# Kernel optimization log

Measured on AMD Instinct MI355X. Metric: run time of the kernel, lower is better.

The kernel has to match this reference:

```python
import jax, jax.numpy as jnp
import numpy as np

N_NODES = 50000
N_EDGES = 625000
D = 128          # hidden_dim
H = 8            # num_heads
DH = D // H      # head_dim
L = 4            # num_layers
F_IN = 64        # in_channels
G = 64           # num graphs
BETA = 1.0
EPS = 1e-5       # layernorm eps


def _seg_softmax(s, idx, n):
    # softmax of s over segments defined by idx (segments present in idx are never empty)
    m = jax.ops.segment_max(s, idx, num_segments=n)
    e = jnp.exp(s - m[idx])
    d = jax.ops.segment_sum(e, idx, num_segments=n)
    return e / d[idx]


def _ln(x, s, b):
    mu = jnp.mean(x, axis=-1, keepdims=True)
    var = jnp.var(x, axis=-1, keepdims=True)
    return (x - mu) / jnp.sqrt(var + EPS) * s + b


def _forward(x, edge_index, batch, node_W, node_b, cW1, cb1, cW2, cb2,
             qW, qb, kW, kb, vW, vb, oW, ob, bW, bb,
             f1W, f1b, f2W, f2b, n1s, n1b, n2s, n2b,
             outW1, outb1, outW2, outb2):
    N = x.shape[0]
    src, tgt = edge_index[0], edge_index[1]
    h = x @ node_W + node_b                              # [N, D]
    for l in range(L):
        # ---- dynamic curvature (attention-approximated Wasserstein) ----
        h_src, h_tgt = h[src], h[tgt]                    # [E, D]
        sim = jnp.sum(h_src * h_tgt, axis=-1) * BETA     # [E]
        alpha = _seg_softmax(sim, tgt, N)                # segment softmax over tgt
        dist = jnp.linalg.norm(h_src - h_tgt, axis=-1)   # [E]
        agg = jax.ops.segment_sum(alpha * dist, tgt, num_segments=N)
        curv = 1.0 - agg[tgt] / jnp.maximum(dist, 1e-6)  # [E]
        ce = jax.nn.relu(curv[:, None] @ cW1 + cb1) @ cW2 + cb2  # [E, D]
        # ---- CurvphormerLayer ----
        xn = _ln(h, n1s[l], n1b[l])
        q = (xn @ qW[l] + qb[l]).reshape(N, H, DH)
        k = (xn @ kW[l] + kb[l]).reshape(N, H, DH)
        v = (xn @ vW[l] + vb[l]).reshape(N, H, DH)
        scores = jnp.sum(q[src] * k[tgt], axis=-1) / (DH ** 0.5)  # [E, H]
        scores = scores + ce @ bW[l] + bb[l]                       # curvature bias
        probs = _seg_softmax(scores, tgt, N)                       # [E, H]
        msgs = (probs[..., None] * v[tgt]).reshape(-1, D)          # [E, D]
        aggm = jax.ops.segment_sum(msgs, src, num_segments=N)     # scatter to src
        h = h + (aggm @ oW[l] + ob[l])
        xn2 = _ln(h, n2s[l], n2b[l])
        h = h + (jax.nn.relu(xn2 @ f1W[l] + f1b[l]) @ f2W[l] + f2b[l])
    # ---- mean pool per graph ----
    counts = jnp.maximum(jax.ops.segment_sum(jnp.ones((N,), h.dtype), batch, num_segments=G), 1.0)
    g = jax.ops.segment_sum(h, batch, num_segments=G) / counts[:, None]
    return jax.nn.relu(g @ outW1 + outb1) @ outW2 + outb2


def setup_inputs() -> dict:
    keys = iter(jax.random.split(jax.random.key(0), 32))
    p = lambda shape, s=0.02: jax.random.normal(next(keys), shape, jnp.float32) * s
    x = jax.random.normal(next(keys), (N_NODES, F_IN), jnp.float32)
    edge_index = jax.random.randint(next(keys), (2, N_EDGES), 0, N_NODES)
    batch = jnp.sort(jax.random.randint(next(keys), (N_NODES,), 0, G))
    inp = {
        "x": x, "edge_index": edge_index, "batch": batch,
        "node_W": p((F_IN, D)), "node_b": p((D,)),
        "cW1": p((1, D)), "cb1": p((D,)), "cW2": p((D, D)), "cb2": p((D,)),
        "qW": p((L, D, D)), "qb": p((L, D)),
        "kW": p((L, D, D)), "kb": p((L, D)),
        "vW": p((L, D, D)), "vb": p((L, D)),
        "oW": p((L, D, D)), "ob": p((L, D)),
        "bW": p((L, D, H)), "bb": p((L, H)),
        "f1W": p((L, D, 4 * D)), "f1b": p((L, 4 * D)),
        "f2W": p((L, 4 * D, D)), "f2b": p((L, D)),
        "n1s": jnp.ones((L, D), jnp.float32), "n1b": jnp.zeros((L, D), jnp.float32),
        "n2s": jnp.ones((L, D), jnp.float32), "n2b": jnp.zeros((L, D), jnp.float32),
        "outW1": p((D, D // 2)), "outb1": p((D // 2,)),
        "outW2": p((D // 2, 1)), "outb2": p((1,)),
    }
    return inp


def reference(x, edge_index, batch, node_W, node_b, cW1, cb1, cW2, cb2,
              qW, qb, kW, kb, vW, vb, oW, ob, bW, bb,
              f1W, f1b, f2W, f2b, n1s, n1b, n2s, n2b,
              outW1, outb1, outW2, outb2):
    return _forward(x, edge_index, batch, node_W, node_b, cW1, cb1, cW2, cb2,
                    qW, qb, kW, kb, vW, vb, oW, ob, bW, bb,
                    f1W, f1b, f2W, f2b, n1s, n1b, n2s, n2b,
                    outW1, outb1, outW2, outb2)
```

## Files before the change

kernel.cpp:

```cpp
#include <hip/hip_runtime.h>

#define NN 50000
#define NE 625000
#define DD 128
#define HH 8
#define DHH 16
#define NL 4
#define FIN 64
#define NG 64
#define LN_EPS 1e-5f
#define NSEG 129
#define NT32 1563
#define NT64 782
#define NT4 12500
#define NBS 196
#define HLP 132

typedef __bf16 bf16x8_t __attribute__((ext_vector_type(8)));
typedef unsigned short ushort8_t __attribute__((ext_vector_type(8)));
typedef float f32x4_t __attribute__((ext_vector_type(4)));
union BF8 { ushort8_t u; bf16x8_t b; };

__device__ __forceinline__ void fma4(float4& a, float s, float4 w) {
  a.x = fmaf(s, w.x, a.x); a.y = fmaf(s, w.y, a.y);
  a.z = fmaf(s, w.z, a.z); a.w = fmaf(s, w.w, a.w);
}
__device__ __forceinline__ unsigned short f2bf(float f) {
  unsigned u = __float_as_uint(f);
  unsigned r = ((u >> 16) & 1u) + 0x7FFFu;
  return (unsigned short)((u + r) >> 16);
}
__device__ __forceinline__ float bf2f(unsigned short u) {
  return __uint_as_float((unsigned)u << 16);
}

__device__ __forceinline__ void ln_tile_bf32(const float* __restrict__ h, int nb,
                                             const float* __restrict__ sc,
                                             const float* __restrict__ bi,
                                             ushort* xbf) {
  int tid = threadIdx.x;
  int r = tid >> 4, l16 = tid & 15;
  int nr = nb + r; if (nr >= NN) nr = NN - 1;
  const float* hp = h + (size_t)nr * DD + l16 * 8;
  float4 a0 = *(const float4*)hp;
  float4 a1 = *(const float4*)(hp + 4);
  float sum = a0.x + a0.y + a0.z + a0.w + a1.x + a1.y + a1.z + a1.w;
  float sq  = a0.x*a0.x + a0.y*a0.y + a0.z*a0.z + a0.w*a0.w
            + a1.x*a1.x + a1.y*a1.y + a1.z*a1.z + a1.w*a1.w;
#pragma unroll
  for (int off = 8; off >= 1; off >>= 1) {
    sum += __shfl_xor(sum, off, 64);
    sq  += __shfl_xor(sq,  off, 64);
  }
  float mu   = sum * (1.0f / DD);
  float var  = sq * (1.0f / DD) - mu * mu;
  float rstd = rsqrtf(var + LN_EPS);
  int d0 = l16 * 8;
  float4 s0 = *(const float4*)(sc + d0), s1 = *(const float4*)(sc + d0 + 4);
  float4 b0 = *(const float4*)(bi + d0), b1 = *(const float4*)(bi + d0 + 4);
  ushort8_t u;
  u[0] = f2bf((a0.x - mu) * rstd * s0.x + b0.x);
  u[1] = f2bf((a0.y - mu) * rstd * s0.y + b0.y);
  u[2] = f2bf((a0.z - mu) * rstd * s0.z + b0.z);
  u[3] = f2bf((a0.w - mu) * rstd * s0.w + b0.w);
  u[4] = f2bf((a1.x - mu) * rstd * s1.x + b1.x);
  u[5] = f2bf((a1.y - mu) * rstd * s1.y + b1.y);
  u[6] = f2bf((a1.z - mu) * rstd * s1.z + b1.z);
  u[7] = f2bf((a1.w - mu) * rstd * s1.w + b1.w);
  int off = (r * 256 + l16 * 16) ^ ((r & 7) << 4);
  *(ushort8_t*)((char*)xbf + off) = u;
}

__global__ __launch_bounds__(256) void k_node_proj(const float* __restrict__ x,
                                                   const float* __restrict__ W,
                                                   const float* __restrict__ b,
                                                   float* __restrict__ h) {
  __shared__ float Wl[FIN * DD];
  __shared__ float xt[32][FIN];
  int tid = threadIdx.x;
  int nb = blockIdx.x * 32;
  for (int i = tid * 4; i < FIN * DD; i += 1024)
    *(float4*)&Wl[i] = *(const float4*)(W + i);
  for (int i = tid * 4; i < 32 * FIN; i += 1024) {
    int row = i >> 6, cc = i & 63;
    int node = nb + row; if (node >= NN) node = NN - 1;
    *(float4*)&xt[row][cc] = *(const float4*)(x + (size_t)node * FIN + cc);
  }
  __syncthreads();
  int c4 = (tid & 31) * 4;
  int r0 = (tid >> 5) * 4;
  float4 bv = *(const float4*)(b + c4);
  float4 a0 = bv, a1 = bv, a2 = bv, a3 = bv;
  for (int k = 0; k < FIN; k++) {
    float4 wv = *(const float4*)&Wl[k * DD + c4];
    fma4(a0, xt[r0][k], wv);
    fma4(a1, xt[r0 + 1][k], wv);
// ... 130 lines not shown
    den += __shfl_xor(den, off, 64);
    nd  += __shfl_xor(nd,  off, 64);
  }
  float av = den > 0.f ? nd / den : 0.f;
  int hh = lane & 7;
  int eidx = lane >> 3;
  const ushort8_t* kp = (const ushort8_t*)(k + (size_t)node * DD + hh * DHH);
  ushort8_t k0 = kp[0], k1 = kp[1];
  float m = -3.4e38f, ssum = 0.f;
  for (int i = rs + eidx; i < re; i += 8) {
    int e = eid_t[i];
    int s = src_s[e];
    float dd = dist[e];
    const ushort8_t* qp = (const ushort8_t*)(q + (size_t)s * DD + hh * DHH);
    ushort8_t q0 = qp[0], q1 = qp[1];
    float curv = 1.0f - av / fmaxf(dd, 1e-6f);
    int lo = 0, hi = DD;
    while (lo < hi) { int mid = (lo + hi) >> 1; if (bp[mid] < curv) lo = mid + 1; else hi = mid; }
    float bias = fmaf(lsl[lo * HH + hh], curv, lin[lo * HH + hh]);
    float dot = 0.f;
#pragma unroll
    for (int jj = 0; jj < 8; jj++) dot = fmaf(bf2f(q0[jj]), bf2f(k0[jj]), dot);
#pragma unroll
    for (int jj = 0; jj < 8; jj++) dot = fmaf(bf2f(q1[jj]), bf2f(k1[jj]), dot);
    float sc = dot * 0.25f + bias;
    escore[e * HH + hh] = sc;
    float mn = fmaxf(m, sc);
    ssum = ssum * expf(m - mn) + expf(sc - mn);
    m = mn;
  }
#pragma unroll
  for (int off = 8; off <= 32; off <<= 1) {
    float m2 = __shfl_xor(m, off, 64);
    float s2 = __shfl_xor(ssum, off, 64);
    float M = fmaxf(m, m2);
    ssum = ssum * expf(m - M) + s2 * expf(m2 - M);
    m = M;
  }
  float inv = ssum > 0.f ? 1.0f / ssum : 0.f;
  for (int i = rs + eidx; i < re; i += 8) {
    size_t idx = (size_t)eid_t[i] * HH + hh;
    float sc = escore[idx];
    escore[idx] = expf(sc - m) * inv;
  }
}

__global__ __launch_bounds__(256) void k_agg(const int* __restrict__ tgt_s,
    const int* __restrict__ rowstart,
    const float* __restrict__ escore,
    const ushort* __restrict__ v, ushort* __restrict__ aggmb) {
  int wave = (blockIdx.x * 256 + threadIdx.x) >> 6;
  int lane = threadIdx.x & 63;
  int rs = rowstart[wave], re = rowstart[wave + 1];
  int hh = lane >> 3;
  int d = lane * 2;
  float a0 = 0.f, a1 = 0.f;
  int i = rs;
  for (; i + 4 <= re; i += 4) {
    int t0 = tgt_s[i], t1 = tgt_s[i + 1], t2 = tgt_s[i + 2], t3 = tgt_s[i + 3];
    float p0 = escore[(i    ) * HH + hh];
    float p1 = escore[(i + 1) * HH + hh];
    float p2 = escore[(i + 2) * HH + hh];
    float p3 = escore[(i + 3) * HH + hh];
    ushort2 v0 = *(const ushort2*)(v + (size_t)t0 * DD + d);
    ushort2 v1 = *(const ushort2*)(v + (size_t)t1 * DD + d);
    ushort2 v2 = *(const ushort2*)(v + (size_t)t2 * DD + d);
    ushort2 v3 = *(const ushort2*)(v + (size_t)t3 * DD + d);
    a0 = fmaf(p0, bf2f(v0.x), a0); a1 = fmaf(p0, bf2f(v0.y), a1);
    a0 = fmaf(p1, bf2f(v1.x), a0); a1 = fmaf(p1, bf2f(v1.y), a1);
    a0 = fmaf(p2, bf2f(v2.x), a0); a1 = fmaf(p2, bf2f(v2.y), a1);
    a0 = fmaf(p3, bf2f(v3.x), a0); a1 = fmaf(p3, bf2f(v3.y), a1);
  }
  for (; i < re; i++) {
    int t = tgt_s[i];
    float prob = escore[i * HH + hh];
    ushort2 vv = *(const ushort2*)(v + (size_t)t * DD + d);
    a0 = fmaf(prob, bf2f(vv.x), a0);
    a1 = fmaf(prob, bf2f(vv.y), a1);
  }
  ushort2 o; o.x = f2bf(a0); o.y = f2bf(a1);
  *(ushort2*)(aggmb + (size_t)wave * DD + d) = o;
}

__global__ __launch_bounds__(512) void k_attn_ffn(const ushort* __restrict__ aggmb,
    const ushort* __restrict__ oT_l, const float* __restrict__ ob_l,
    const float* __restrict__ n2s_l, const float* __restrict__ n2b_l,
    const ushort* __restrict__ f1T_l, const float* __restrict__ f1b_l,
    const ushort* __restrict__ f2T_l, const float* __restrict__ f2b_l,
    float* __restrict__ h,
    int do_qkv,
    const float* __restrict__ n1s_n, const float* __restrict__ n1b_n,
    const ushort* __restrict__ qkvT_n,
    const float* __restrict__ qb_n, const float* __restrict__ kb_n, const float* __restrict__ vb_n,
    ushort* __restrict__ q, ushort* __restrict__ kk, ushort* __restrict__ v) {
  __shared__ float hL[64 * HLP];
  __shared__ __align__(16) char ubuf[64 * 128 * 2];
  char* xb = ubuf;
  char* tb = ubuf;
  int nb = blockIdx.x * 64;
  int tid = threadIdx.x;
  int lane = tid & 63, w = tid >> 6;
  int g = lane >> 4, c = lane & 15;
  int colb = w * 16;
  int xr = (c & 7) << 4;
  {
    float4 obv = *(const float4*)(ob_l + colb + g * 4);
    const ushort* wp = oT_l + (size_t)(colb + c) * DD + g * 8;
    BF8 b0, b1, b2, b3;
    b0.u = *(const ushort8_t*)(wp);
    b1.u = *(const ushort8_t*)(wp + 32);
    b2.u = *(const ushort8_t*)(wp + 64);
    b3.u = *(const ushort8_t*)(wp + 96);
#pragma unroll
    for (int nt = 0; nt < 4; nt++) {
      int node = nb + nt * 16 + c;
      int na = node < NN ? node : NN - 1;
      const ushort* ap = aggmb + (size_t)na * DD + g * 8;
      BF8 a0, a1, a2, a3;
      a0.u = *(const ushort8_t*)(ap);
      a1.u = *(const ushort8_t*)(ap + 32);
      a2.u = *(const ushort8_t*)(ap + 64);
      a3.u = *(const ushort8_t*)(ap + 96);
      f32x4_t acc = {obv.x, obv.y, obv.z, obv.w};
      acc = __builtin_amdgcn_mfma_f32_16x16x32_bf16(b0.b, a0.b, acc, 0, 0, 0);
      acc = __builtin_amdgcn_mfma_f32_16x16x32_bf16(b1.b, a1.b, acc, 0, 0, 0);
      acc = __builtin_amdgcn_mfma_f32_16x16x32_bf16(b2.b, a2.b, acc, 0, 0, 0);
      acc = __builtin_amdgcn_mfma_f32_16x16x32_bf16(b3.b, a3.b, acc, 0, 0, 0);
      float4 hv = *(const float4*)(h + (size_t)na * DD + colb + g * 4);
      hv.x += acc[0]; hv.y += acc[1]; hv.z += acc[2]; hv.w += acc[3];
      *(float4*)&hL[(nt * 16 + c) * HLP + colb + g * 4] = hv;
    }
  }
  __syncthreads();
  {
    int l16 = tid & 15;
    int d0 = l16 * 8;
    float4 s0 = *(const float4*)(n2s_l + d0), s1 = *(const float4*)(n2s_l + d0 + 4);
    float4 bb0 = *(const float4*)(n2b_l + d0), bb1 = *(const float4*)(n2b_l + d0 + 4);
#pragma unroll
    for (int p = 0; p < 2; p++) {
      int r = p * 32 + (tid >> 4);
      const float* hp = &hL[r * HLP + d0];
      float4 a0 = *(const float4*)hp;
      float4 a1 = *(const float4*)(hp + 4);
      float sum = a0.x + a0.y + a0.z + a0.w + a1.x + a1.y + a1.z + a1.w;
      float sq  = a0.x*a0.x + a0.y*a0.y + a0.z*a0.z + a0.w*a0.w
                + a1.x*a1.x + a1.y*a1.y + a1.z*a1.z + a1.w*a1.w;
#pragma unroll
      for (int off = 8; off >= 1; off >>= 1) {
        sum += __shfl_xor(sum, off, 64);
        sq  += __shfl_xor(sq,  off, 64);
      }
      float mu   = sum * (1.0f / DD);
      float var  = sq * (1.0f / DD) - mu * mu;
      float rstd = rsqrtf(var + LN_EPS);
      ushort8_t u;
      u[0] = f2bf((a0.x - mu) * rstd * s0.x + bb0.x);
      u[1] = f2bf((a0.y - mu) * rstd * s0.y + bb0.y);
      u[2] = f2bf((a0.z - mu) * rstd * s0.z + bb0.z);
      u[3] = f2bf((a0.w - mu) * rstd * s0.w + bb0.w);
      u[4] = f2bf((a1.x - mu) * rstd * s1.x + bb1.x);
      u[5] = f2bf((a1.y - mu) * rstd * s1.y + bb1.y);
      u[6] = f2bf((a1.z - mu) * rstd * s1.z + bb1.z);
      u[7] = f2bf((a1.w - mu) * rstd * s1.w + bb1.w);
      int off = (r * 256 + l16 * 16) ^ ((r & 7) << 4);
      *(ushort8_t*)(xb + off) = u;
    }
  }
  __syncthreads();
  BF8 a[4][4];
#pragma unroll
  for (int nt = 0; nt < 4; nt++)
#pragma unroll
    for (int kt = 0; kt < 4; kt++)
      a[nt][kt].u = *(ushort8_t*)(xb + (((nt * 16 + c) * 256 + kt * 64 + g * 16) ^ xr));
  __syncthreads();
  float4 bv2 = *(const float4*)(f2b_l + colb + g * 4);
  f32x4_t o0 = {bv2.x, bv2.y, bv2.z, bv2.w};
  f32x4_t o1 = o0, o2 = o0, o3 = o0;
#pragma unroll
  for (int ch = 0; ch < 4; ch++) {
    if (ch) __syncthreads();
    {
      int col = ch * 128 + w * 16;
      float4 bv = *(const float4*)(f1b_l + col + g * 4);
      f32x4_t ac0 = {bv.x, bv.y, bv.z, bv.w};
      f32x4_t ac1 = ac0, ac2 = ac0, ac3 = ac0;
      const ushort* wp = f1T_l + (size_t)(col + c) * DD + g * 8;
#pragma unroll
      for (int kt = 0; kt < 4; kt++) {
        BF8 b; b.u = *(const ushort8_t*)(wp + kt * 32);
        ac0 = __builtin_amdgcn_mfma_f32_16x16x32_bf16(b.b, a[0][kt].b, ac0, 0, 0, 0);
        ac1 = __builtin_amdgcn_mfma_f32_16x16x32_bf16(b.b, a[1][kt].b, ac1, 0, 0, 0);
        ac2 = __builtin_amdgcn_mfma_f32_16x16x32_bf16(b.b, a[2][kt].b, ac2, 0, 0, 0);
        ac3 = __builtin_amdgcn_mfma_f32_16x16x32_bf16(b.b, a[3][kt].b, ac3, 0, 0, 0);
      }
      int colL = (w * 16 + g * 4) * 2;
      {
        int row = c;
        ushort4 o4; o4.x = f2bf(fmaxf(ac0[0], 0.f)); o4.y = f2bf(fmaxf(ac0[1], 0.f));
        o4.z = f2bf(fmaxf(ac0[2], 0.f)); o4.w = f2bf(fmaxf(ac0[3], 0.f));
        *(ushort4*)(tb + ((row * 256 + colL) ^ ((row & 7) << 4))) = o4;
      }
      {
        int row = 16 + c;
        ushort4 o4; o4.x = f2bf(fmaxf(ac1[0], 0.f)); o4.y = f2bf(fmaxf(ac1[1], 0.f));
        o4.z = f2bf(fmaxf(ac1[2], 0.f)); o4.w = f2bf(fmaxf(ac1[3], 0.f));
        *(ushort4*)(tb + ((row * 256 + colL) ^ ((row & 7) << 4))) = o4;
      }
      {
        int row = 32 + c;
        ushort4 o4; o4.x = f2bf(fmaxf(ac2[0], 0.f)); o4.y = f2bf(fmaxf(ac2[1], 0.f));
        o4.z = f2bf(fmaxf(ac2[2], 0.f)); o4.w = f2bf(fmaxf(ac2[3], 0.f));
        *(ushort4*)(tb + ((row * 256 + colL) ^ ((row & 7) << 4))) = o4;
      }
      {
        int row = 48 + c;
        ushort4 o4; o4.x = f2bf(fmaxf(ac3[0], 0.f)); o4.y = f2bf(fmaxf(ac3[1], 0.f));
        o4.z = f2bf(fmaxf(ac3[2], 0.f)); o4.w = f2bf(fmaxf(ac3[3], 0.f));
        *(ushort4*)(tb + ((row * 256 + colL) ^ ((row & 7) << 4))) = o4;
      }
    }
    __syncthreads();
    const ushort* wp2 = f2T_l + (size_t)(colb + c) * 512 + ch * 128 + g * 8;
#pragma unroll
    for (int kt = 0; kt < 4; kt++) {
      BF8 b; b.u = *(const ushort8_t*)(wp2 + kt * 32);
      BF8 t0; t0.u = *(ushort8_t*)(tb + (((c) * 256 + kt * 64 + g * 16) ^ xr));
      BF8 t1; t1.u = *(ushort8_t*)(tb + (((16 + c) * 256 + kt * 64 + g * 16) ^ xr));
      BF8 t2; t2.u = *(ushort8_t*)(tb + (((32 + c) * 256 + kt * 64 + g * 16) ^ xr));
      BF8 t3; t3.u = *(ushort8_t*)(tb + (((48 + c) * 256 + kt * 64 + g * 16) ^ xr));
      o0 = __builtin_amdgcn_mfma_f32_16x16x32_bf16(b.b, t0.b, o0, 0, 0, 0);
      o1 = __builtin_amdgcn_mfma_f32_16x16x32_bf16(b.b, t1.b, o1, 0, 0, 0);
      o2 = __builtin_amdgcn_mfma_f32_16x16x32_bf16(b.b, t2.b, o2, 0, 0, 0);
      o3 = __builtin_amdgcn_mfma_f32_16x16x32_bf16(b.b, t3.b, o3, 0, 0, 0);
    }
  }
  {
    float* lp = &hL[c * HLP + colb + g * 4];
    float4 hv = *(const float4*)lp;
    hv.x += o0[0]; hv.y += o0[1]; hv.z += o0[2]; hv.w += o0[3];
    *(float4*)lp = hv;
    int node = nb + c;
    if (node < NN) *(float4*)(h + (size_t)node * DD + colb + g * 4) = hv;
  }
  {
    float* lp = &hL[(16 + c) * HLP + colb + g * 4];
    float4 hv = *(const float4*)lp;
    hv.x += o1[0]; hv.y += o1[1]; hv.z += o1[2]; hv.w += o1[3];
    *(float4*)lp = hv;
    int node = nb + 16 + c;
    if (node < NN) *(float4*)(h + (size_t)node * DD + colb + g * 4) = hv;
  }
  {
    float* lp = &hL[(32 + c) * HLP + colb + g * 4];
    float4 hv = *(const float4*)lp;
    hv.x += o2[0]; hv.y += o2[1]; hv.z += o2[2]; hv.w += o2[3];
    *(float4*)lp = hv;
    int node = nb + 32 + c;
    if (node < NN) *(float4*)(h + (size_t)node * DD + colb + g * 4) = hv;
  }
  {
    float* lp = &hL[(48 + c) * HLP + colb + g * 4];
    float4 hv = *(const float4*)lp;
    hv.x += o3[0]; hv.y += o3[1]; hv.z += o3[2]; hv.w += o3[3];
    *(float4*)lp = hv;
    int node = nb + 48 + c;
    if (node < NN) *(float4*)(h + (size_t)node * DD + colb + g * 4) = hv;
  }
  if (!do_qkv) return;
  __syncthreads();
  {
    int l16 = tid & 15;
    int d0 = l16 * 8;
    float4 s0 = *(const float4*)(n1s_n + d0), s1 = *(const float4*)(n1s_n + d0 + 4);
    float4 bb0 = *(const float4*)(n1b_n + d0), bb1 = *(const float4*)(n1b_n + d0 + 4);
#pragma unroll
    for (int p = 0; p < 2; p++) {
      int r = p * 32 + (tid >> 4);
      const float* hp = &hL[r * HLP + d0];
      float4 a0 = *(const float4*)hp;
      float4 a1 = *(const float4*)(hp + 4);
      float sum = a0.x + a0.y + a0.z + a0.w + a1.x + a1.y + a1.z + a1.w;
      float sq  = a0.x*a0.x + a0.y*a0.y + a0.z*a0.z + a0.w*a0.w
                + a1.x*a1.x + a1.y*a1.y + a1.z*a1.z + a1.w*a1.w;
#pragma unroll
      for (int off = 8; off >= 1; off >>= 1) {
        sum += __shfl_xor(sum, off, 64);
        sq  += __shfl_xor(sq,  off, 64);
      }
      float mu   = sum * (1.0f / DD);
      float var  = sq * (1.0f / DD) - mu * mu;
      float rstd = rsqrtf(var + LN_EPS);
      ushort8_t u;
      u[0] = f2bf((a0.x - mu) * rstd * s0.x + bb0.x);
      u[1] = f2bf((a0.y - mu) * rstd * s0.y + bb0.y);
      u[2] = f2bf((a0.z - mu) * rstd * s0.z + bb0.z);
      u[3] = f2bf((a0.w - mu) * rstd * s0.w + bb0.w);
      u[4] = f2bf((a1.x - mu) * rstd * s1.x + bb1.x);
      u[5] = f2bf((a1.y - mu) * rstd * s1.y + bb1.y);
      u[6] = f2bf((a1.z - mu) * rstd * s1.z + bb1.z);
      u[7] = f2bf((a1.w - mu) * rstd * s1.w + bb1.w);
      int off = (r * 256 + l16 * 16) ^ ((r & 7) << 4);
      *(ushort8_t*)(xb + off) = u;
    }
  }
  __syncthreads();
  BF8 aq[4][4];
#pragma unroll
  for (int nt = 0; nt < 4; nt++)
#pragma unroll
    for (int kt = 0; kt < 4; kt++)
      aq[nt][kt].u = *(ushort8_t*)(xb + (((nt * 16 + c) * 256 + kt * 64 + g * 16) ^ xr));
#pragma unroll
  for (int ti = 0; ti < 3; ti++) {
    int t = w * 3 + ti;
    int m = t >> 3;
    int colq = (t & 7) * 16;
    const float* bias = (m == 0 ? qb_n : (m == 1 ? kb_n : vb_n));
    float4 bv = *(const float4*)(bias + colq + g * 4);
    f32x4_t ac0 = {bv.x, bv.y, bv.z, bv.w};
    f32x4_t ac1 = ac0, ac2 = ac0, ac3 = ac0;
    const ushort* wp = qkvT_n + (size_t)(m * DD + colq + c) * DD + g * 8;
#pragma unroll
    for (int kt = 0; kt < 4; kt++) {
      BF8 b; b.u = *(const ushort8_t*)(wp + kt * 32);
      ac0 = __builtin_amdgcn_mfma_f32_16x16x32_bf16(b.b, aq[0][kt].b, ac0, 0, 0, 0);
      ac1 = __builtin_amdgcn_mfma_f32_16x16x32_bf16(b.b, aq[1][kt].b, ac1, 0, 0, 0);
      ac2 = __builtin_amdgcn_mfma_f32_16x16x32_bf16(b.b, aq[2][kt].b, ac2, 0, 0, 0);
      ac3 = __builtin_amdgcn_mfma_f32_16x16x32_bf16(b.b, aq[3][kt].b, ac3, 0, 0, 0);
    }
    ushort* out = (m == 0 ? q : (m == 1 ? kk : v));
    {
      int node = nb + c;
      if (node < NN) {
        ushort4 o; o.x = f2bf(ac0[0]); o.y = f2bf(ac0[1]); o.z = f2bf(ac0[2]); o.w = f2bf(ac0[3]);
        *(ushort4*)(out + (size_t)node * DD + colq + g * 4) = o;
      }
    }
    {
      int node = nb + 16 + c;
      if (node < NN) {
        ushort4 o; o.x = f2bf(ac1[0]); o.y = f2bf(ac1[1]); o.z = f2bf(ac1[2]); o.w = f2bf(ac1[3]);
        *(ushort4*)(out + (size_t)node * DD + colq + g * 4) = o;
      }
    }
    {
      int node = nb + 32 + c;
      if (node < NN) {
        ushort4 o; o.x = f2bf(ac2[0]); o.y = f2bf(ac2[1]); o.z = f2bf(ac2[2]); o.w = f2bf(ac2[3]);
        *(ushort4*)(out + (size_t)node * DD + colq + g * 4) = o;
      }
    }
    {
      int node = nb + 48 + c;
      if (node < NN) {
        ushort4 o; o.x = f2bf(ac3[0]); o.y = f2bf(ac3[1]); o.z = f2bf(ac3[2]); o.w = f2bf(ac3[3]);
        *(ushort4*)(out + (size_t)node * DD + colq + g * 4) = o;
      }
    }
  }
}

__global__ __launch_bounds__(256) void k_zero(int* __restrict__ cnt, int* __restrict__ cur,
                                              int* __restrict__ cnt_t, int* __restrict__ cur_t,
                                              int* __restrict__ gstart, int* __restrict__ gend,
                                              float* __restrict__ gpool) {
  int i = blockIdx.x * 256 + threadIdx.x;
  if (i < NN) { cnt[i] = 0; cur[i] = 0; cnt_t[i] = 0; cur_t[i] = 0; }
  if (i < NG) { gstart[i] = 0; gend[i] = 0; }
  if (i < NG * DD) gpool[i] = 0.f;
}

__global__ void k_hist2(const int* __restrict__ src, const int* __restrict__ tgt,
                        int* __restrict__ cnt, int* __restrict__ cnt_t) {
  int e = blockIdx.x * 256 + threadIdx.x;
  if (e < NE) {
    atomicAdd(cnt + src[e], 1);
    atomicAdd(cnt_t + tgt[e], 1);
  }
}

__global__ __launch_bounds__(256) void k_scan_blk2(const int* __restrict__ cnt,
                                                   const int* __restrict__ cnt_t,
                                                   int* __restrict__ bsum, int* __restrict__ bsum_t) {
  __shared__ int red[256];
  int arr = blockIdx.x >= NBS ? 1 : 0;
  int b = blockIdx.x - arr * NBS;
  const int* c = arr ? cnt_t : cnt;
  int* bs = arr ? bsum_t : bsum;
  int tid = threadIdx.x;
  int idx = b * 256 + tid;
  red[tid] = (idx < NN) ? c[idx] : 0;
  __syncthreads();
  for (int off = 128; off >= 1; off >>= 1) {
    if (tid < off) red[tid] += red[tid + off];
    __syncthreads();
  }
  if (tid == 0) bs[b] = red[0];
}

__global__ __launch_bounds__(256) void k_scan_top2(const int* __restrict__ bsum,
                                                   const int* __restrict__ bsum_t,
                                                   int* __restrict__ boff, int* __restrict__ boff_t,
                                                   int* __restrict__ rowstart, int* __restrict__ rowstart_t) {
  __shared__ int ps[256];
  int arr = blockIdx.x;
  const int* bs = arr ? bsum_t : bsum;
  int* bo = arr ? boff_t : boff;
  int* rsN = arr ? rowstart_t : rowstart;
  int t = threadIdx.x;
  int v = (t < NBS) ? bs[t] : 0;
  ps[t] = v;
  __syncthreads();
  for (int off = 1; off < 256; off <<= 1) {
    int x = (t >= off) ? ps[t - off] : 0;
    __syncthreads();
    ps[t] += x;
    __syncthreads();
  }
  bo[t] = ps[t] - v;
  if (t == 255) rsN[NN] = ps[255];
}

__global__ __launch_bounds__(256) void k_scan_fin2(const int* __restrict__ cnt,
                                                   const int* __restrict__ cnt_t,
                                                   const int* __restrict__ boff, const int* __restrict__ boff_t,
                                                   int* __restrict__ rowstart, int* __restrict__ rowstart_t) {
  __shared__ int ps[256];
  int arr = blockIdx.x >= NBS ? 1 : 0;
  int b = blockIdx.x - arr * NBS;
  const int* c = arr ? cnt_t : cnt;
  const int* bo = arr ? boff_t : boff;
  int* rs = arr ? rowstart_t : rowstart;
  int t = threadIdx.x;
  int idx = b * 256 + t;
  int v = (idx < NN) ? c[idx] : 0;
  ps[t] = v;
  __syncthreads();
  for (int off = 1; off < 256; off <<= 1) {
    int x = (t >= off) ? ps[t - off] : 0;
    __syncthreads();
    ps[t] += x;
    __syncthreads();
  }
  if (idx < NN) rs[idx] = bo[b] + ps[t] - v;
}

__global__ void k_fill(const int* __restrict__ src, const int* __restrict__ tgt,
                       const int* __restrict__ rowstart,
                       int* __restrict__ cur, int* __restrict__ src_s, int* __restrict__ tgt_s) {
  int e = blockIdx.x * 256 + threadIdx.x;
  if (e >= NE) return;
// ... 37 lines not shown
  idx -= SZ1;
  if (idx < SZF) { wt_one(f1W, f1T, idx, DD, 512, DD * 512); return; }
  idx -= SZF;
  if (idx < SZF) { wt_one(f2W, f2T, idx, 512, DD, 512 * DD); return; }
}

__global__ __launch_bounds__(64) void k_mbias_par(const float* __restrict__ cW2, const float* __restrict__ cb2,
                                                  const float* __restrict__ bW, const float* __restrict__ bb,
                                                  float* __restrict__ M, float* __restrict__ base) {
  int bid = blockIdx.x;
  int l = bid >> 7, d = bid & 127;
  int lane = threadIdx.x;
  int hh = lane >> 3, j0 = lane & 7;
  const float* bWl = bW + (size_t)l * DD * HH;
  float acc = 0.f;
#pragma unroll
  for (int t = 0; t < 16; t++) {
    int k = j0 + t * 8;
    acc = fmaf(cW2[d * DD + k], bWl[k * HH + hh], acc);
  }
#pragma unroll
  for (int off = 1; off <= 4; off <<= 1) acc += __shfl_xor(acc, off, 64);
  if (j0 == 0) M[(size_t)l * DD * HH + d * HH + hh] = acc;
  if (d == 0) {
    float bacc = 0.f;
#pragma unroll
    for (int t = 0; t < 16; t++) {
      int k = j0 + t * 8;
      bacc = fmaf(cb2[k], bWl[k * HH + hh], bacc);
    }
#pragma unroll
    for (int off = 1; off <= 4; off <<= 1) bacc += __shfl_xor(bacc, off, 64);
    if (j0 == 0) base[l * HH + hh] = bacc + bb[l * HH + hh];
  }
}

__global__ __launch_bounds__(128) void k_bp(const float* __restrict__ cW1, const float* __restrict__ cb1,
                                            float* __restrict__ bpg, int* __restrict__ posg) {
  __shared__ float x[DD], bp[DD];
  int tid = threadIdx.x;
  float c1v = cW1[tid], cbv = cb1[tid];
  x[tid] = (c1v == 0.f) ? __builtin_inff() : (-cbv / c1v);
  __syncthreads();
  float xv = x[tid]; int p = 0;
  for (int j = 0; j < DD; j++) {
    float xj = x[j];
    if (xj < xv || (xj == xv && j < tid)) p++;
  }
  bp[p] = xv;
  posg[tid] = p;
  __syncthreads();
  bpg[tid] = bp[tid];
}

__global__ __launch_bounds__(64) void k_pwl_tab(const float* __restrict__ cW1, const float* __restrict__ cb1,
    const int* __restrict__ posg, const float* __restrict__ Mb, const float* __restrict__ basel,
    float* __restrict__ slopeg, float* __restrict__ interg) {
  int bid = blockIdx.x;
  int l = bid / NSEG, s = bid - l * NSEG;
  int lane = threadIdx.x;
  int hh = lane >> 3, j0 = lane & 7;
  const float* M = Mb + (size_t)l * DD * HH;
  float sl = 0.f, in = 0.f;
#pragma unroll
  for (int t = 0; t < 16; t++) {
    int d = j0 + t * 8;
    float cv = cW1[d], cbv = cb1[d];
    int p = posg[d];
    bool act = (cv == 0.f) ? (cbv > 0.f) : ((cv > 0.f) ? (p < s) : (p >= s));
    float m = act ? M[d * HH + hh] : 0.f;
    sl = fmaf(cv, m, sl);
    in = fmaf(cbv, m, in);
  }
#pragma unroll
  for (int off = 1; off <= 4; off <<= 1) {
    sl += __shfl_xor(sl, off, 64);
    in += __shfl_xor(in, off, 64);
  }
  if (j0 == 0) {
    size_t o = (size_t)l * NSEG * HH + s * HH + hh;
    slopeg[o] = sl;
    interg[o] = in + basel[l * HH + hh];
  }
}

__global__ void k_bounds(const int* __restrict__ batch, int* __restrict__ gstart, int* __restrict__ gend) {
  int n = blockIdx.x * 256 + threadIdx.x;
  if (n >= NN) return;
  int b = batch[n];
  if (n == 0 || batch[n - 1] != b) gstart[b] = n;
  if (n == NN - 1 || batch[n + 1] != b) gend[b] = n + 1;
}

__global__ __launch_bounds__(256) void k_pool_part(const float* __restrict__ h,
    const int* __restrict__ batch, float* __restrict__ gpool) {
  int tid = threadIdx.x;
  int d = tid & 127, sub = tid >> 7;
  int n0 = blockIdx.x * 256;
  int nend = n0 + 256; if (nend > NN) nend = NN;
  float run = 0.f; int gcur = -1;
  for (int n = n0 + sub; n < nend; n += 2) {
    int g = batch[n];
    if (g != gcur) {
      if (gcur >= 0) atomicAdd(gpool + (size_t)gcur * DD + d, run);
      run = 0.f; gcur = g;
    }
    run += h[(size_t)n * DD + d];
  }
  if (gcur >= 0) atomicAdd(gpool + (size_t)gcur * DD + d, run);
}

__global__ __launch_bounds__(256) void k_head(const float* __restrict__ gpool,
    const int* __restrict__ gstart, const int* __restrict__ gend,
    const float* __restrict__ W1, const float* __restrict__ b1,
    const float* __restrict__ W2, const float* __restrict__ b2, float* __restrict__ out) {
  __shared__ float mid[NG * 64];
  int tid = threadIdx.x;
  for (int idx = tid; idx < NG * 64; idx += 256) {
    int g = idx >> 6, j = idx & 63;
    int cnt = gend[g] - gstart[g]; if (cnt < 1) cnt = 1;
    float rc = 1.0f / (float)cnt;
    float acc = 0.f;
    for (int d = 0; d < DD; d++) acc = fmaf(gpool[g * DD + d], W1[d * 64 + j], acc);
    mid[idx] = fmaxf(fmaf(acc, rc, b1[j]), 0.f);
  }
  __syncthreads();
  if (tid < NG) {
    float acc = b2[0];
    for (int j = 0; j < 64; j++) acc = fmaf(mid[tid * 64 + j], W2[j], acc);
    out[tid] = acc;
  }
}

extern "C" void kernel_launch(void* const* d_in, const int* in_sizes, int n_in,
                              void* d_out, int out_size, void* d_ws, size_t ws_size,
                              hipStream_t stream) {
  const float* x      = (const float*)d_in[0];
  const int*   ei     = (const int*)d_in[1];
  const int*   batch  = (const int*)d_in[2];
  const float* node_W = (const float*)d_in[3];
  const float* node_b = (const float*)d_in[4];
  const float* cW1    = (const float*)d_in[5];
  const float* cb1    = (const float*)d_in[6];
  const float* cW2    = (const float*)d_in[7];
  const float* cb2    = (const float*)d_in[8];
  const float* qW     = (const float*)d_in[9];
  const float* qb     = (const float*)d_in[10];
  const float* kW     = (const float*)d_in[11];
  const float* kb     = (const float*)d_in[12];
  const float* vW     = (const float*)d_in[13];
  const float* vb     = (const float*)d_in[14];
  const float* oW     = (const float*)d_in[15];
  const float* ob     = (const float*)d_in[16];
  const float* bW     = (const float*)d_in[17];
  const float* bb     = (const float*)d_in[18];
  const float* f1W    = (const float*)d_in[19];
  const float* f1b    = (const float*)d_in[20];
  const float* f2W    = (const float*)d_in[21];
  const float* f2b    = (const float*)d_in[22];
  const float* n1s    = (const float*)d_in[23];
  const float* n1b    = (const float*)d_in[24];
  const float* n2s    = (const float*)d_in[25];
  const float* n2b    = (const float*)d_in[26];
  const float* outW1  = (const float*)d_in[27];
  const float* outb1  = (const float*)d_in[28];
  const float* outW2  = (const float*)d_in[29];
  const float* outb2  = (const float*)d_in[30];

  const int* src = ei;
  const int* tgt = ei + NE;

  char* wp = (char*)d_ws;
  auto alloc = [&](size_t bytes) { void* p = (void*)wp; wp += (bytes + 255) & ~(size_t)255; return p; };
  float*    h       = (float*)alloc((size_t)NN * DD * 4);
  ushort*   q       = (ushort*)alloc((size_t)NN * DD * 2);
  ushort*   kk      = (ushort*)alloc((size_t)NN * DD * 2);
  ushort*   v       = (ushort*)alloc((size_t)NN * DD * 2);
  ushort*   aggmb   = (ushort*)alloc((size_t)NN * DD * 2);
  float*    sim     = (float*)alloc((size_t)NE * 4);
  float*    dist    = (float*)alloc((size_t)NE * 4);
  float*    escore  = (float*)alloc((size_t)NE * HH * 4);
  float*    Mb      = (float*)alloc((size_t)NL * DD * HH * 4);
  float*    basel   = (float*)alloc((size_t)NL * HH * 4);
  float*    bpg     = (float*)alloc((size_t)DD * 4);
  int*      posg    = (int*)alloc((size_t)DD * 4);
  float*    slopeg  = (float*)alloc((size_t)NL * NSEG * HH * 4);
  float*    interg  = (float*)alloc((size_t)NL * NSEG * HH * 4);
  int*      rowstart= (int*)alloc((size_t)(NN + 1) * 4);
  int*      rowstart_t = (int*)alloc((size_t)(NN + 1) * 4);
  int*      eid_t   = (int*)alloc((size_t)NE * 4);
  int*      src_s   = (int*)alloc((size_t)NE * 4);
  int*      tgt_s   = (int*)alloc((size_t)NE * 4);
  int*      cnt     = (int*)alloc((size_t)NN * 4);
  int*      cur     = (int*)alloc((size_t)NN * 4);
  int*      cnt_t   = (int*)alloc((size_t)NN * 4);
  int*      cur_t   = (int*)alloc((size_t)NN * 4);
  int*      bsum    = (int*)alloc((size_t)NBS * 4);
  int*      bsum_t  = (int*)alloc((size_t)NBS * 4);
  int*      boff    = (int*)alloc((size_t)256 * 4);
  int*      boff_t  = (int*)alloc((size_t)256 * 4);
  int*      gstart  = (int*)alloc((size_t)NG * 4);
  int*      gend    = (int*)alloc((size_t)NG * 4);
  float*    gpool   = (float*)alloc((size_t)NG * DD * 4);
  ushort*   qkvT    = (ushort*)alloc((size_t)NL * 3 * DD * DD * 2);
  ushort*   oT      = (ushort*)alloc((size_t)NL * DD * DD * 2);
  ushort*   f1T     = (ushort*)alloc((size_t)NL * DD * 512 * 2);
  ushort*   f2T     = (ushort*)alloc((size_t)NL * 512 * DD * 2);
  (void)in_sizes; (void)n_in; (void)out_size; (void)ws_size;

  k_zero<<<NBS, 256, 0, stream>>>(cnt, cur, cnt_t, cur_t, gstart, gend, gpool);
  k_hist2<<<(NE + 255) / 256, 256, 0, stream>>>(src, tgt, cnt, cnt_t);
  k_scan_blk2<<<2 * NBS, 256, 0, stream>>>(cnt, cnt_t, bsum, bsum_t);
  k_scan_top2<<<2, 256, 0, stream>>>(bsum, bsum_t, boff, boff_t, rowstart, rowstart_t);
  k_scan_fin2<<<2 * NBS, 256, 0, stream>>>(cnt, cnt_t, boff, boff_t, rowstart, rowstart_t);
  k_fill<<<(NE + 255) / 256, 256, 0, stream>>>(src, tgt, rowstart, cur, src_s, tgt_s);
  k_fill_t<<<(NE + 255) / 256, 256, 0, stream>>>(tgt_s, rowstart_t, cur_t, eid_t);
  k_mbias_par<<<NL * DD, 64, 0, stream>>>(cW2, cb2, bW, bb, Mb, basel);
  k_bp<<<1, 128, 0, stream>>>(cW1, cb1, bpg, posg);
  k_pwl_tab<<<NL * NSEG, 64, 0, stream>>>(cW1, cb1, posg, Mb, basel, slopeg, interg);
  k_bounds<<<(NN + 255) / 256, 256, 0, stream>>>(batch, gstart, gend);
  k_wt_all<<<(4 * NL * DD * DD + 2 * NL * DD * 512 + 255) / 256, 256, 0, stream>>>(
      qW, kW, vW, oW, f1W, f2W, qkvT, oT, f1T, f2T);
  k_node_proj<<<NT32, 256, 0, stream>>>(x, node_W, node_b, h);
  k_ln_qkv<<<NT32, 512, 0, stream>>>(h, n1s, n1b, qkvT, qb, kb, vb, q, kk, v);

  for (int l = 0; l < NL; l++) {
    k_edge1<<<(NE * 8 + 255) / 256, 256, 0, stream>>>(src_s, tgt_s, h, sim, dist);
    k_scores_sm<<<NT4, 256, 0, stream>>>(src_s, rowstart_t, eid_t, q, kk,
        sim, dist, bpg,
        slopeg + (size_t)l * NSEG * HH, interg + (size_t)l * NSEG * HH,
        escore);
    k_agg<<<NN / 4, 256, 0, stream>>>(tgt_s, rowstart, escore, v, aggmb);
    int ln = l < NL - 1 ? l + 1 : l;
    k_attn_ffn<<<NT64, 512, 0, stream>>>(aggmb, oT + (size_t)l * DD * DD, ob + l * DD,
        n2s + l * DD, n2b + l * DD,
        f1T + (size_t)l * DD * 512, f1b + (size_t)l * 4 * DD,
        f2T + (size_t)l * 512 * DD, f2b + l * DD, h,
        (l < NL - 1) ? 1 : 0,
        n1s + ln * DD, n1b + ln * DD,
        qkvT + (size_t)ln * 3 * DD * DD,
        qb + ln * DD, kb + ln * DD, vb + ln * DD,
        q, kk, v);
  }
  k_pool_part<<<(NN + 255) / 256, 256, 0, stream>>>(h, batch, gpool);
  k_head<<<1, 256, 0, stream>>>(gpool, gstart, gend, outW1, outb1, outW2, outb2, (float*)d_out);
}
```

Measured before the change: 1.279 ms.

## Shrink attn-FFN tile to 32 nodes with 4 waves each owning two column tiles

The fused attention-output/LN/FFN/QKV kernel now processes 32 nodes per block with 256 threads instead of 64 nodes with 512 threads. Each wave covers two 16-column tiles and only two node subtiles, which halves LDS use and A-fragment registers and doubles the grid size. The aim is higher occupancy and better load balance across CUs, at the cost of loading each weight fragment for fewer nodes and so issuing more weight traffic overall. Separately, the graph-bounds computation is folded into the zero-init kernel, removing one launch.

Result: no change. 1.274 ms (median of 2 runs) (-0.4%).

```diff
diff --git a/kernel.cpp b/kernel.cpp
--- a/kernel.cpp
+++ b/kernel.cpp
@@ -11,7 +11,6 @@
 #define LN_EPS 1e-5f
 #define NSEG 129
 #define NT32 1563
-#define NT64 782
 #define NT4 12500
 #define NBS 196
 #define HLP 132
@@ -308,7 +307,7 @@
   *(ushort2*)(aggmb + (size_t)wave * DD + d) = o;
 }
 
-__global__ __launch_bounds__(512) void k_attn_ffn(const ushort* __restrict__ aggmb,
+__global__ __launch_bounds__(256) void k_attn_ffn(const ushort* __restrict__ aggmb,
     const ushort* __restrict__ oT_l, const float* __restrict__ ob_l,
     const float* __restrict__ n2s_l, const float* __restrict__ n2b_l,
     const ushort* __restrict__ f1T_l, const float* __restrict__ f1b_l,
@@ -319,17 +318,19 @@
     const ushort* __restrict__ qkvT_n,
     const float* __restrict__ qb_n, const float* __restrict__ kb_n, const float* __restrict__ vb_n,
     ushort* __restrict__ q, ushort* __restrict__ kk, ushort* __restrict__ v) {
-  __shared__ float hL[64 * HLP];
-  __shared__ __align__(16) char ubuf[64 * 128 * 2];
+  __shared__ float hL[32 * HLP];
+  __shared__ __align__(16) char ubuf[32 * 128 * 2];
   char* xb = ubuf;
   char* tb = ubuf;
-  int nb = blockIdx.x * 64;
+  int nb = blockIdx.x * 32;
   int tid = threadIdx.x;
   int lane = tid & 63, w = tid >> 6;
   int g = lane >> 4, c = lane & 15;
-  int colb = w * 16;
   int xr = (c & 7) << 4;
-  {
+  int colb0 = (w * 2) * 16, colb1 = (w * 2 + 1) * 16;
+#pragma unroll
+  for (int ti = 0; ti < 2; ti++) {
+    int colb = (w * 2 + ti) * 16;
     float4 obv = *(const float4*)(ob_l + colb + g * 4);
     const ushort* wp = oT_l + (size_t)(colb + c) * DD + g * 8;
     BF8 b0, b1, b2, b3;
@@ -338,7 +339,7 @@
     b2.u = *(const ushort8_t*)(wp + 64);
     b3.u = *(const ushort8_t*)(wp + 96);
 #pragma unroll
-    for (int nt = 0; nt < 4; nt++) {
+    for (int nt = 0; nt < 2; nt++) {
       int node = nb + nt * 16 + c;
       int na = node < NN ? node : NN - 1;
       const ushort* ap = aggmb + (size_t)na * DD + g * 8;
@@ -365,7 +366,7 @@
     float4 bb0 = *(const float4*)(n2b_l + d0), bb1 = *(const float4*)(n2b_l + d0 + 4);
 #pragma unroll
     for (int p = 0; p < 2; p++) {
-      int r = p * 32 + (tid >> 4);
+      int r = p * 16 + (tid >> 4);
       const float* hp = &hL[r * HLP + d0];
       float4 a0 = *(const float4*)hp;
       float4 a1 = *(const float4*)(hp + 4);
@@ -394,34 +395,36 @@
     }
   }
   __syncthreads();
-  BF8 a[4][4];
-#pragma unroll
-  for (int nt = 0; nt < 4; nt++)
+  BF8 a[2][4];
+#pragma unroll
+  for (int nt = 0; nt < 2; nt++)
 #pragma unroll
     for (int kt = 0; kt < 4; kt++)
       a[nt][kt].u = *(ushort8_t*)(xb + (((nt * 16 + c) * 256 + kt * 64 + g * 16) ^ xr));
   __syncthreads();
-  float4 bv2 = *(const float4*)(f2b_l + colb + g * 4);
-  f32x4_t o0 = {bv2.x, bv2.y, bv2.z, bv2.w};
-  f32x4_t o1 = o0, o2 = o0, o3 = o0;
+  float4 bv20 = *(const float4*)(f2b_l + colb0 + g * 4);
+  float4 bv21 = *(const float4*)(f2b_l + colb1 + g * 4);
+  f32x4_t o00 = {bv20.x, bv20.y, bv20.z, bv20.w};
+  f32x4_t o01 = o00;
+  f32x4_t o10 = {bv21.x, bv21.y, bv21.z, bv21.w};
+  f32x4_t o11 = o10;
 #pragma unroll
   for (int ch = 0; ch < 4; ch++) {
     if (ch) __syncthreads();
-    {
-      int col = ch * 128 + w * 16;
+#pragma unroll
+    for (int ti = 0; ti < 2; ti++) {
+      int col = ch * 128 + (w * 2 + ti) * 16;
       float4 bv = *(const float4*)(f1b_l + col + g * 4);
       f32x4_t ac0 = {bv.x, bv.y, bv.z, bv.w};
-      f32x4_t ac1 = ac0, ac2 = ac0, ac3 = ac0;
+      f32x4_t ac1 = ac0;
       const ushort* wp = f1T_l + (size_t)(col + c) * DD + g * 8;
 #pragma unroll
       for (int kt = 0; kt < 4; kt++) {
         BF8 b; b.u = *(const ushort8_t*)(wp + kt * 32);
         ac0 = __builtin_amdgcn_mfma_f32_16x16x32_bf16(b.b, a[0][kt].b, ac0, 0, 0, 0);
         ac1 = __builtin_amdgcn_mfma_f32_16x16x32_bf16(b.b, a[1][kt].b, ac1, 0, 0, 0);
-        ac2 = __builtin_amdgcn_mfma_f32_16x16x32_bf16(b.b, a[2][kt].b, ac2, 0, 0, 0);
-        ac3 = __builtin_amdgcn_mfma_f32_16x16x32_bf16(b.b, a[3][kt].b, ac3, 0, 0, 0);
       }
-      int colL = (w * 16 + g * 4) * 2;
+      int colL = ((w * 2 + ti) * 16 + g * 4) * 2;
       {
         int row = c;
         ushort4 o4; o4.x = f2bf(fmaxf(ac0[0], 0.f)); o4.y = f2bf(fmaxf(ac0[1], 0.f));
@@ -434,65 +437,53 @@
         o4.z = f2bf(fmaxf(ac1[2], 0.f)); o4.w = f2bf(fmaxf(ac1[3], 0.f));
         *(ushort4*)(tb + ((row * 256 + colL) ^ ((row & 7) << 4))) = o4;
       }
-      {
-        int row = 32 + c;
-        ushort4 o4; o4.x = f2bf(fmaxf(ac2[0], 0.f)); o4.y = f2bf(fmaxf(ac2[1], 0.f));
-        o4.z = f2bf(fmaxf(ac2[2], 0.f)); o4.w = f2bf(fmaxf(ac2[3], 0.f));
-        *(ushort4*)(tb + ((row * 256 + colL) ^ ((row & 7) << 4))) = o4;
-      }
-      {
-        int row = 48 + c;
-        ushort4 o4; o4.x = f2bf(fmaxf(ac3[0], 0.f)); o4.y = f2bf(fmaxf(ac3[1], 0.f));
-        o4.z = f2bf(fmaxf(ac3[2], 0.f)); o4.w = f2bf(fmaxf(ac3[3], 0.f));
-        *(ushort4*)(tb + ((row * 256 + colL) ^ ((row & 7) << 4))) = o4;
-      }
     }
     __syncthreads();
-    const ushort* wp2 = f2T_l + (size_t)(colb + c) * 512 + ch * 128 + g * 8;
+    const ushort* wp20 = f2T_l + (size_t)(colb0 + c) * 512 + ch * 128 + g * 8;
+    const ushort* wp21 = f2T_l + (size_t)(colb1 + c) * 512 + ch * 128 + g * 8;
 #pragma unroll
     for (int kt = 0; kt < 4; kt++) {
-      BF8 b; b.u = *(const ushort8_t*)(wp2 + kt * 32);
       BF8 t0; t0.u = *(ushort8_t*)(tb + (((c) * 256 + kt * 64 + g * 16) ^ xr));
       BF8 t1; t1.u = *(ushort8_t*)(tb + (((16 + c) * 256 + kt * 64 + g * 16) ^ xr));
-      BF8 t2; t2.u = *(ushort8_t*)(tb + (((32 + c) * 256 + kt * 64 + g * 16) ^ xr));
-      BF8 t3; t3.u = *(ushort8_t*)(tb + (((48 + c) * 256 + kt * 64 + g * 16) ^ xr));
-      o0 = __builtin_amdgcn_mfma_f32_16x16x32_bf16(b.b, t0.b, o0, 0, 0, 0);
-      o1 = __builtin_amdgcn_mfma_f32_16x16x32_bf16(b.b, t1.b, o1, 0, 0, 0);
-      o2 = __builtin_amdgcn_mfma_f32_16x16x32_bf16(b.b, t2.b, o2, 0, 0, 0);
-      o3 = __builtin_amdgcn_mfma_f32_16x16x32_bf16(b.b, t3.b, o3, 0, 0, 0);
+      BF8 bA; bA.u = *(const ushort8_t*)(wp20 + kt * 32);
+      o00 = __builtin_amdgcn_mfma_f32_16x16x32_bf16(bA.b, t0.b, o00, 0, 0, 0);
+      o01 = __builtin_amdgcn_mfma_f32_16x16x32_bf16(bA.b, t1.b, o01, 0, 0, 0);
+      BF8 bB; bB.u = *(const ushort8_t*)(wp21 + kt * 32);
+      o10 = __builtin_amdgcn_mfma_f32_16x16x32_bf16(bB.b, t0.b, o10, 0, 0, 0);
+      o11 = __builtin_amdgcn_mfma_f32_16x16x32_bf16(bB.b, t1.b, o11, 0, 0, 0);
     }
   }
   {
-    float* lp = &hL[c * HLP + colb + g * 4];
+    float* lp = &hL[c * HLP + colb0 + g * 4];
     float4 hv = *(const float4*)lp;
-    hv.x += o0[0]; hv.y += o0[1]; hv.z += o0[2]; hv.w += o0[3];
+    hv.x += o00[0]; hv.y += o00[1]; hv.z += o00[2]; hv.w += o00[3];
     *(float4*)lp = hv;
     int node = nb + c;
-    if (node < NN) *(float4*)(h + (size_t)node * DD + colb + g * 4) = hv;
+    if (node < NN) *(float4*)(h + (size_t)node * DD + colb0 + g * 4) = hv;
   }
   {
-    float* lp = &hL[(16 + c) * HLP + colb + g * 4];
+    float* lp = &hL[(16 + c) * HLP + colb0 + g * 4];
     float4 hv = *(const float4*)lp;
-    hv.x += o1[0]; hv.y += o1[1]; hv.z += o1[2]; hv.w += o1[3];
+    hv.x += o01[0]; hv.y += o01[1]; hv.z += o01[2]; hv.w += o01[3];
     *(float4*)lp = hv;
     int node = nb + 16 + c;
-    if (node < NN) *(float4*)(h + (size_t)node * DD + colb + g * 4) = hv;
+    if (node < NN) *(float4*)(h + (size_t)node * DD + colb0 + g * 4) = hv;
   }
   {
-    float* lp = &hL[(32 + c) * HLP + colb + g * 4];
+    float* lp = &hL[c * HLP + colb1 + g * 4];
     float4 hv = *(const float4*)lp;
-    hv.x += o2[0]; hv.y += o2[1]; hv.z += o2[2]; hv.w += o2[3];
+    hv.x += o10[0]; hv.y += o10[1]; hv.z += o10[2]; hv.w += o10[3];
     *(float4*)lp = hv;
-    int node = nb + 32 + c;
-    if (node < NN) *(float4*)(h + (size_t)node * DD + colb + g * 4) = hv;
+    int node = nb + c;
+    if (node < NN) *(float4*)(h + (size_t)node * DD + colb1 + g * 4) = hv;
   }
   {
-    float* lp = &hL[(48 + c) * HLP + colb + g * 4];
+    float* lp = &hL[(16 + c) * HLP + colb1 + g * 4];
     float4 hv = *(const float4*)lp;
-    hv.x += o3[0]; hv.y += o3[1]; hv.z += o3[2]; hv.w += o3[3];
+    hv.x += o11[0]; hv.y += o11[1]; hv.z += o11[2]; hv.w += o11[3];
     *(float4*)lp = hv;
-    int node = nb + 48 + c;
-    if (node < NN) *(float4*)(h + (size_t)node * DD + colb + g * 4) = hv;
+    int node = nb + 16 + c;
+    if (node < NN) *(float4*)(h + (size_t)node * DD + colb1 + g * 4) = hv;
   }
   if (!do_qkv) return;
   __syncthreads();
@@ -503,7 +494,7 @@
     float4 bb0 = *(const float4*)(n1b_n + d0), bb1 = *(const float4*)(n1b_n + d0 + 4);
 #pragma unroll
     for (int p = 0; p < 2; p++) {
-      int r = p * 32 + (tid >> 4);
+      int r = p * 16 + (tid >> 4);
       const float* hp = &hL[r * HLP + d0];
       float4 a0 = *(const float4*)hp;
       float4 a1 = *(const float4*)(hp + 4);
@@ -532,29 +523,27 @@
     }
   }
   __syncthreads();
-  BF8 aq[4][4];
-#pragma unroll
-  for (int nt = 0; nt < 4; nt++)
+  BF8 aq[2][4];
+#pragma unroll
+  for (int nt = 0; nt < 2; nt++)
 #pragma unroll
     for (int kt = 0; kt < 4; kt++)
       aq[nt][kt].u = *(ushort8_t*)(xb + (((nt * 16 + c) * 256 + kt * 64 + g * 16) ^ xr));
 #pragma unroll
-  for (int ti = 0; ti < 3; ti++) {
-    int t = w * 3 + ti;
+  for (int ti = 0; ti < 6; ti++) {
+    int t = w * 6 + ti;
     int m = t >> 3;
     int colq = (t & 7) * 16;
     const float* bias = (m == 0 ? qb_n : (m == 1 ? kb_n : vb_n));
     float4 bv = *(const float4*)(bias + colq + g * 4);
     f32x4_t ac0 = {bv.x, bv.y, bv.z, bv.w};
-    f32x4_t ac1 = ac0, ac2 = ac0, ac3 = ac0;
+    f32x4_t ac1 = ac0;
     const ushort* wp = qkvT_n + (size_t)(m * DD + colq + c) * DD + g * 8;
 #pragma unroll
     for (int kt = 0; kt < 4; kt++) {
       BF8 b; b.u = *(const ushort8_t*)(wp + kt * 32);
       ac0 = __builtin_amdgcn_mfma_f32_16x16x32_bf16(b.b, aq[0][kt].b, ac0, 0, 0, 0);
       ac1 = __builtin_amdgcn_mfma_f32_16x16x32_bf16(b.b, aq[1][kt].b, ac1, 0, 0, 0);
-      ac2 = __builtin_amdgcn_mfma_f32_16x16x32_bf16(b.b, aq[2][kt].b, ac2, 0, 0, 0);
-      ac3 = __builtin_amdgcn_mfma_f32_16x16x32_bf16(b.b, aq[3][kt].b, ac3, 0, 0, 0);
     }
     ushort* out = (m == 0 ? q : (m == 1 ? kk : v));
     {
@@ -571,30 +560,21 @@
         *(ushort4*)(out + (size_t)node * DD + colq + g * 4) = o;
       }
     }
-    {
-      int node = nb + 32 + c;
-      if (node < NN) {
-        ushort4 o; o.x = f2bf(ac2[0]); o.y = f2bf(ac2[1]); o.z = f2bf(ac2[2]); o.w = f2bf(ac2[3]);
-        *(ushort4*)(out + (size_t)node * DD + colq + g * 4) = o;
-      }
-    }
-    {
-      int node = nb + 48 + c;
-      if (node < NN) {
-        ushort4 o; o.x = f2bf(ac3[0]); o.y = f2bf(ac3[1]); o.z = f2bf(ac3[2]); o.w = f2bf(ac3[3]);
-        *(ushort4*)(out + (size_t)node * DD + colq + g * 4) = o;
-      }
-    }
   }
 }
 
 __global__ __launch_bounds__(256) void k_zero(int* __restrict__ cnt, int* __restrict__ cur,
                                               int* __restrict__ cnt_t, int* __restrict__ cur_t,
+                                              const int* __restrict__ batch,
                                               int* __restrict__ gstart, int* __restrict__ gend,
                                               float* __restrict__ gpool) {
   int i = blockIdx.x * 256 + threadIdx.x;
-  if (i < NN) { cnt[i] = 0; cur[i] = 0; cnt_t[i] = 0; cur_t[i] = 0; }
-  if (i < NG) { gstart[i] = 0; gend[i] = 0; }
+  if (i < NN) {
+    cnt[i] = 0; cur[i] = 0; cnt_t[i] = 0; cur_t[i] = 0;
+    int b = batch[i];
+    if (i == 0 || batch[i - 1] != b) gstart[b] = i;
+    if (i == NN - 1 || batch[i + 1] != b) gend[b] = i + 1;
+  }
   if (i < NG * DD) gpool[i] = 0.f;
 }
 
@@ -798,14 +778,6 @@
     slopeg[o] = sl;
     interg[o] = in + basel[l * HH + hh];
   }
-}
-
-__global__ void k_bounds(const int* __restrict__ batch, int* __restrict__ gstart, int* __restrict__ gend) {
-  int n = blockIdx.x * 256 + threadIdx.x;
-  if (n >= NN) return;
-  int b = batch[n];
-  if (n == 0 || batch[n - 1] != b) gstart[b] = n;
-  if (n == NN - 1 || batch[n + 1] != b) gend[b] = n + 1;
 }
 
 __global__ __launch_bounds__(256) void k_pool_part(const float* __restrict__ h,
@@ -924,7 +896,7 @@
   ushort*   f2T     = (ushort*)alloc((size_t)NL * 512 * DD * 2);
   (void)in_sizes; (void)n_in; (void)out_size; (void)ws_size;
 
-  k_zero<<<NBS, 256, 0, stream>>>(cnt, cur, cnt_t, cur_t, gstart, gend, gpool);
+  k_zero<<<NBS, 256, 0, stream>>>(cnt, cur, cnt_t, cur_t, batch, gstart, gend, gpool);
   k_hist2<<<(NE + 255) / 256, 256, 0, stream>>>(src, tgt, cnt, cnt_t);
   k_scan_blk2<<<2 * NBS, 256, 0, stream>>>(cnt, cnt_t, bsum, bsum_t);
   k_scan_top2<<<2, 256, 0, stream>>>(bsum, bsum_t, boff, boff_t, rowstart, rowstart_t);
@@ -934,7 +906,6 @@
   k_mbias_par<<<NL * DD, 64, 0, stream>>>(cW2, cb2, bW, bb, Mb, basel);
   k_bp<<<1, 128, 0, stream>>>(cW1, cb1, bpg, posg);
   k_pwl_tab<<<NL * NSEG, 64, 0, stream>>>(cW1, cb1, posg, Mb, basel, slopeg, interg);
-  k_bounds<<<(NN + 255) / 256, 256, 0, stream>>>(batch, gstart, gend);
   k_wt_all<<<(4 * NL * DD * DD + 2 * NL * DD * 512 + 255) / 256, 256, 0, stream>>>(
       qW, kW, vW, oW, f1W, f2W, qkvT, oT, f1T, f2T);
   k_node_proj<<<NT32, 256, 0, stream>>>(x, node_W, node_b, h);
@@ -948,7 +919,7 @@
         escore);
     k_agg<<<NN / 4, 256, 0, stream>>>(tgt_s, rowstart, escore, v, aggmb);
     int ln = l < NL - 1 ? l + 1 : l;
-    k_attn_ffn<<<NT64, 512, 0, stream>>>(aggmb, oT + (size_t)l * DD * DD, ob + l * DD,
+    k_attn_ffn<<<NT32, 256, 0, stream>>>(aggmb, oT + (size_t)l * DD * DD, ob + l * DD,
         n2s + l * DD, n2b + l * DD,
         f1T + (size_t)l * DD * 512, f1b + (size_t)l * 4 * DD,
         f2T + (size_t)l * 512 * DD, f2b + l * DD, h,
```
